# Kernel optimization log

Hardware: AMD Instinct MI355X
Metric: run time of the kernel (lower is better)

The kernel has to match this reference:

```python
import jax, jax.numpy as jnp
import numpy as np

# Dimensions (see shape_source)
B, N, F = 2, 400, 246          # batch, nodes, node features
S = 1                           # edge feature channels
C = 32                          # stack_channels
LBL = 1440                      # shape_node_labels
STACK_IN = 2 * F + 2 * S        # concat([x_i, x_j, e_ij, e_ji])
NODE_IN = F + 2 * C             # concat([x, agg_in, agg_out])


def _glorot(key, shape):
    fan_in, fan_out = shape[0], shape[1]
    lim = np.sqrt(6.0 / (fan_in + fan_out)).astype(np.float32)
    return jax.random.uniform(key, shape, jnp.float32, -lim, lim)


def setup_inputs() -> dict:
    key = jax.random.key(0)
    ks = jax.random.split(key, 12)
    x = jax.random.normal(ks[0], (B, N, F), jnp.float32)
    a = (jax.random.uniform(ks[1], (B, N, N)) < 0.10).astype(jnp.float32)
    e = jax.random.uniform(ks[2], (B, N, N, S), jnp.float32)
    return {
        "x": x,
        "a": a,
        "e": e,
        # XENetConv stack model: single Dense(C) + PReLU (per-channel alpha)
        "W_stack": _glorot(ks[3], (STACK_IN, C)),
        "b_stack": jnp.zeros((C,), jnp.float32),
        "alpha": jnp.full((C,), 0.25, jnp.float32),
        # attention heads: Dense(1, sigmoid) each
        "W_att_i": _glorot(ks[4], (C, 1)),
        "b_att_i": jnp.zeros((1,), jnp.float32),
        "W_att_j": _glorot(ks[5], (C, 1)),
        "b_att_j": jnp.zeros((1,), jnp.float32),
        # node model: Dense(F) over concat([x, agg_in, agg_out]) (linear)
        "W_node": _glorot(ks[6], (NODE_IN, F)),
        "b_node": jnp.zeros((F,), jnp.float32),
        # trailing Dense(shape_node_labels, linear)
        "W_out": _glorot(ks[7], (F, LBL)),
        "b_out": jnp.zeros((LBL,), jnp.float32),
    }


def reference(x, a, e, W_stack, b_stack, alpha, W_att_i, b_att_i,
              W_att_j, b_att_j, W_node, b_node, W_out, b_out):
    # --- XENetConvBatch ---
    # pairwise stack: [x_i, x_j, e_ij, e_ji] over all (i, j) node pairs
    x_i = jnp.broadcast_to(x[:, :, None, :], (B, N, N, F))
    x_j = jnp.broadcast_to(x[:, None, :, :], (B, N, N, F))
    e_t = jnp.transpose(e, (0, 2, 1, 3))                     # e_ji
    stack = jnp.concatenate([x_i, x_j, e, e_t], axis=-1)     # (B,N,N,2F+2S)
    s = jnp.einsum("bijk,kc->bijc", stack, W_stack) + b_stack  # (B,N,N,C)
    s = jnp.where(s >= 0, s, alpha * s)                      # PReLU
    s = s * a[..., None]                                     # mask non-edges
    # attention (sigmoid gates for incoming / outgoing aggregation)
    att_i = jax.nn.sigmoid(s @ W_att_i + b_att_i)            # (B,N,N,1)
    att_j = jax.nn.sigmoid(s @ W_att_j + b_att_j)
    agg_i = jnp.sum(s * att_i, axis=2)                       # (B,N,C) sum over j
    agg_j = jnp.sum(s * att_j, axis=1)                       # (B,N,C) sum over i
    x_new = jnp.concatenate([x, agg_i, agg_j], axis=-1) @ W_node + b_node  # (B,N,F)
    # Net discards the edge output of the conv; final linear Dense
    out = x_new @ W_out + b_out                              # (B,N,LBL)
    return out
```

## Files before the change

kernel.cpp:

```cpp
#include <hip/hip_runtime.h>
#include <math.h>

#define B_ 2
#define N_ 400
#define F_ 246
#define C_ 32
#define LBL_ 1440
#define NODE_IN_ 310

#define KX_ 320
#define KN_ 256

#define T_ABUF (800 * KX_)
#define T_WNT  (256 * KX_)
#define T_WOT  (LBL_ * KN_)

typedef __attribute__((ext_vector_type(8))) short bf16x8;
typedef __attribute__((ext_vector_type(4))) float f32x4;

__device__ __forceinline__ short f2bf(float f) {
    unsigned u = __float_as_uint(f);
    return (short)((u + 0x7FFF + ((u >> 16) & 1)) >> 16);
}

template <int K>
__device__ __forceinline__ f32x4 mfma_tile(const short* __restrict__ A,
                                           const short* __restrict__ BT,
                                           int m0, int n0, int lane) {
    int r = lane & 15, quad = lane >> 4;
    const short* ap = A + (size_t)(m0 + r) * K + quad * 8;
    const short* bp = BT + (size_t)(n0 + r) * K + quad * 8;
    f32x4 acc = {0.f, 0.f, 0.f, 0.f};
    #pragma unroll
    for (int kk = 0; kk < K; kk += 32) {
        bf16x8 av = *(const bf16x8*)(ap + kk);
        bf16x8 bv = *(const bf16x8*)(bp + kk);
        acc = __builtin_amdgcn_mfma_f32_16x16x32_bf16(av, bv, acc, 0, 0, 0);
    }
    return acc;
}

__global__ void k_pre(const float* __restrict__ x, const float* __restrict__ Ws,
                      const float* __restrict__ Wn, const float* __restrict__ Wo,
                      float* __restrict__ PQ, short* __restrict__ Abuf,
                      short* __restrict__ WnT, short* __restrict__ WoT) {
    __shared__ short tile[32][33];
    int bx = blockIdx.x, tid = threadIdx.x;
    if (bx < 50) {
        int w = tid >> 6, lane = tid & 63;
        int m0 = bx * 16, n = w * 16 + (lane & 15);
        int r = lane & 15, quad = lane >> 4;
        const float* xrow = x + (size_t)(m0 + r) * F_;
        f32x4 acc = {0.f, 0.f, 0.f, 0.f};
        #pragma unroll
        for (int kk = 0; kk < 256; kk += 32) {
            int kb = kk + quad * 8;
            bf16x8 av, bv;
            #pragma unroll
            for (int j = 0; j < 8; ++j) {
                int k = kb + j;
                av[j] = (k < F_) ? f2bf(xrow[k]) : (short)0;
                float f = 0.f;
                if (k < F_) f = (n < C_) ? Ws[k * C_ + n]
                                         : Ws[(F_ + k) * C_ + (n - C_)];
                bv[j] = f2bf(f);
            }
            acc = __builtin_amdgcn_mfma_f32_16x16x32_bf16(av, bv, acc, 0, 0, 0);
        }
        int mb = m0 + quad * 4;
        #pragma unroll
        for (int rr = 0; rr < 4; ++rr)
            PQ[(size_t)(mb + rr) * 64 + n] = acc[rr];
        return;
    }
    bx -= 50;
    if (bx < 100) {
        int r0 = bx * 8;
        for (int idx = tid; idx < 8 * F_; idx += 256) {
            int lr = idx / F_, k = idx - lr * F_;
            Abuf[(size_t)(r0 + lr) * KX_ + k] = f2bf(x[(size_t)(r0 + lr) * F_ + k]);
        }
        return;
    }
    bx -= 100;
    int tx = tid & 31, ty = tid >> 5;
    if (bx < 360) {
        int n0 = (bx % 45) * 32, k0 = (bx / 45) * 32;
        #pragma unroll
        for (int r = 0; r < 4; ++r) {
            int k = k0 + ty + r * 8;
            tile[ty + r * 8][tx] = (k < F_) ? f2bf(Wo[k * LBL_ + n0 + tx]) : (short)0;
        }
        __syncthreads();
        #pragma unroll
        for (int r = 0; r < 4; ++r)
            WoT[(size_t)(n0 + ty + r * 8) * KN_ + k0 + tx] = tile[tx][ty + r * 8];
        return;
    }
    bx -= 360;
    {
        int n0 = (bx % 8) * 32, k0 = (bx / 8) * 32;
        #pragma unroll
        for (int r = 0; r < 4; ++r) {
            int k = k0 + ty + r * 8, n = n0 + tx;
            tile[ty + r * 8][tx] =
                (n < F_ && k < NODE_IN_) ? f2bf(Wn[k * F_ + n]) : (short)0;
        }
        __syncthreads();
        #pragma unroll
        for (int r = 0; r < 4; ++r)
            WnT[(size_t)(n0 + ty + r * 8) * KX_ + k0 + tx] = tile[tx][ty + r * 8];
    }
}

__global__ void k_agg(const float* __restrict__ a, const float* __restrict__ e,
                      const float* __restrict__ Ws, const float* __restrict__ bs,
                      const float* __restrict__ alpha,
                      const float* __restrict__ Wai, const float* __restrict__ bai,
                      const float* __restrict__ Waj, const float* __restrict__ baj,
                      const float* __restrict__ PQ, short* __restrict__ Abuf) {
    int blk  = blockIdx.x;
    int mode = (blk >= B_ * N_) ? 1 : 0;
    int row  = mode ? blk - B_ * N_ : blk;
    int b = row / N_, n = row % N_;
    int tid = threadIdx.x;
    int c = tid & 31, g = tid >> 5;

    float w3  = Ws[(2 * F_) * C_ + c];
    float w4  = Ws[(2 * F_ + 1) * C_ + c];
    float bsc = bs[c];
    float alc = alpha[c];
    float wat = mode ? Waj[c] : Wai[c];
    float bat = mode ? baj[0] : bai[0];

    float ownc = PQ[(size_t)row * 64 + (mode ? 32 : 0) + c];
    const float* oth = PQ + (size_t)b * N_ * 64 + (mode ? 0 : 32) + c;
    const float* abase = a + (size_t)b * N_ * N_;
    const float* ebase = e + (size_t)b * N_ * N_;

    float acc = 0.f;
    #pragma unroll 4
    for (int m = g; m < N_; m += 8) {
        float aij  = mode ? abase[m * N_ + n] : abase[n * N_ + m];
        float er   = ebase[n * N_ + m];
        float ec   = ebase[m * N_ + n];
        float othv = oth[(size_t)m * 64];
        if (aij != 0.f) {
            float eij = mode ? ec : er;
            float eji = mode ? er : ec;
            float raw = ownc + othv + eij * w3 + eji * w4 + bsc;
            float s = (raw >= 0.f ? raw : alc * raw) * aij;
            float t2 = s * wat;
            t2 += __shfl_xor(t2, 1, 32);
            t2 += __shfl_xor(t2, 2, 32);
            t2 += __shfl_xor(t2, 4, 32);
            t2 += __shfl_xor(t2, 8, 32);
            t2 += __shfl_xor(t2, 16, 32);
            float att = 1.f / (1.f + __expf(-(t2 + bat)));
            acc += s * att;
        }
    }
    __shared__ float part[8][C_ + 1];
    part[g][c] = acc;
    __syncthreads();
    if (tid < C_) {
        float tot = 0.f;
        #pragma unroll
        for (int gg = 0; gg < 8; ++gg) tot += part[gg][tid];
        Abuf[(size_t)row * KX_ + F_ + mode * C_ + tid] = f2bf(tot);
    }
}

__global__ __launch_bounds__(1024, 1)
void k_nodeout(const short* __restrict__ Abuf, const short* __restrict__ WnT,
               const float* __restrict__ bn, const short* __restrict__ WoT,
               const float* __restrict__ bo, float* __restrict__ out) {
    __shared__ short Xs[16][264];
    int tid = threadIdx.x;
    int w = tid >> 6, lane = tid & 63;
    int m0 = blockIdx.x * 16;
    int col = lane & 15, quad = lane >> 4;

    {
        int n0 = w * 16;
        f32x4 acc = mfma_tile<KX_>(Abuf, WnT, m0, n0, lane);
        int nn = n0 + col;
        float bv = (nn < F_) ? bn[nn] : 0.f;
        #pragma unroll
        for (int r = 0; r < 4; ++r)
            Xs[quad * 4 + r][nn] = (nn < F_) ? f2bf(acc[r] + bv) : (short)0;
    }
    __syncthreads();

    const short* xbase = &Xs[0][0];
    for (int tt = w; tt < 18; tt += 16) {
        int n0 = (blockIdx.y * 18 + tt) * 16;
        int r = lane & 15;
        const short* ap = xbase + r * 264 + quad * 8;
        const short* bp = WoT + (size_t)(n0 + r) * KN_ + quad * 8;
        f32x4 acc = {0.f, 0.f, 0.f, 0.f};
        #pragma unroll
        for (int kk = 0; kk < KN_; kk += 32) {
            bf16x8 av = *(const bf16x8*)(ap + kk);
            bf16x8 bv = *(const bf16x8*)(bp + kk);
            acc = __builtin_amdgcn_mfma_f32_16x16x32_bf16(av, bv, acc, 0, 0, 0);
        }
        int nn = n0 + col;
        float bv = bo[nn];
        #pragma unroll
        for (int rr = 0; rr < 4; ++rr)
            out[(size_t)(m0 + quad * 4 + rr) * LBL_ + nn] = acc[rr] + bv;
    }
}

extern "C" void kernel_launch(void* const* d_in, const int* in_sizes, int n_in,
                              void* d_out, int out_size, void* d_ws, size_t ws_size,
                              hipStream_t stream) {
    const float* x   = (const float*)d_in[0];
    const float* a   = (const float*)d_in[1];
    const float* e   = (const float*)d_in[2];
    const float* Ws  = (const float*)d_in[3];
    const float* bs  = (const float*)d_in[4];
    const float* al  = (const float*)d_in[5];
    const float* Wai = (const float*)d_in[6];
    const float* bai = (const float*)d_in[7];
    const float* Waj = (const float*)d_in[8];
    const float* baj = (const float*)d_in[9];
    const float* Wn  = (const float*)d_in[10];
    const float* bn  = (const float*)d_in[11];
    const float* Wo  = (const float*)d_in[12];
    const float* bo  = (const float*)d_in[13];

    float* PQ   = (float*)d_ws;
    short* Abuf = (short*)(PQ + 800 * 64);
    short* WnT  = Abuf + T_ABUF;
    short* WoT  = WnT + T_WNT;

    k_pre<<<590, 256, 0, stream>>>(x, Ws, Wn, Wo, PQ, Abuf, WnT, WoT);
    k_agg<<<2 * B_ * N_, 256, 0, stream>>>(a, e, Ws, bs, al, Wai, bai, Waj, baj,
                                           PQ, Abuf);
    k_nodeout<<<dim3(50, 5), 1024, 0, stream>>>(Abuf, WnT, bn, WoT, bo,
                                                (float*)d_out);
}
```

Before: 132.6 us.

## Split PQ projection into separate MFMA kernel and rebalance nodeout tiling

The x·W_stack projection that was computed inside the prep kernel, with per-element bf16 conversion of x and Ws, is moved to a new small MFMA kernel. That kernel reads a pre-transposed bf16 W2T and the bf16 Abuf, both produced by the prep kernel, which now uses one block per row for the x conversion. The output GEMM in k_nodeout is regridded from 5 to 6 column groups with 15 tiles per block, removing the loop in which only two waves worked on the second pass. The cost is an extra kernel launch and an additional dependency between the prep and projection stages.

After: 140.9 us. 1.06x slower.

```diff
diff --git a/kernel.cpp b/kernel.cpp
--- a/kernel.cpp
+++ b/kernel.cpp
@@ -12,6 +12,7 @@
 #define KN_ 256
 
 #define T_ABUF (800 * KX_)
+#define T_W2T  (64 * KX_)
 #define T_WNT  (256 * KX_)
 #define T_WOT  (LBL_ * KN_)
 
@@ -40,49 +41,17 @@
     return acc;
 }
 
-__global__ void k_pre(const float* __restrict__ x, const float* __restrict__ Ws,
-                      const float* __restrict__ Wn, const float* __restrict__ Wo,
-                      float* __restrict__ PQ, short* __restrict__ Abuf,
-                      short* __restrict__ WnT, short* __restrict__ WoT) {
+__global__ void k_prep(const float* __restrict__ x, const float* __restrict__ Ws,
+                       const float* __restrict__ Wn, const float* __restrict__ Wo,
+                       short* __restrict__ Abuf, short* __restrict__ W2T,
+                       short* __restrict__ WnT, short* __restrict__ WoT) {
     __shared__ short tile[32][33];
     int bx = blockIdx.x, tid = threadIdx.x;
-    if (bx < 50) {
-        int w = tid >> 6, lane = tid & 63;
-        int m0 = bx * 16, n = w * 16 + (lane & 15);
-        int r = lane & 15, quad = lane >> 4;
-        const float* xrow = x + (size_t)(m0 + r) * F_;
-        f32x4 acc = {0.f, 0.f, 0.f, 0.f};
-        #pragma unroll
-        for (int kk = 0; kk < 256; kk += 32) {
-            int kb = kk + quad * 8;
-            bf16x8 av, bv;
-            #pragma unroll
-            for (int j = 0; j < 8; ++j) {
-                int k = kb + j;
-                av[j] = (k < F_) ? f2bf(xrow[k]) : (short)0;
-                float f = 0.f;
-                if (k < F_) f = (n < C_) ? Ws[k * C_ + n]
-                                         : Ws[(F_ + k) * C_ + (n - C_)];
-                bv[j] = f2bf(f);
-            }
-            acc = __builtin_amdgcn_mfma_f32_16x16x32_bf16(av, bv, acc, 0, 0, 0);
-        }
-        int mb = m0 + quad * 4;
-        #pragma unroll
-        for (int rr = 0; rr < 4; ++rr)
-            PQ[(size_t)(mb + rr) * 64 + n] = acc[rr];
+    if (bx < 800) {
+        if (tid < F_) Abuf[bx * KX_ + tid] = f2bf(x[bx * F_ + tid]);
         return;
     }
-    bx -= 50;
-    if (bx < 100) {
-        int r0 = bx * 8;
-        for (int idx = tid; idx < 8 * F_; idx += 256) {
-            int lr = idx / F_, k = idx - lr * F_;
-            Abuf[(size_t)(r0 + lr) * KX_ + k] = f2bf(x[(size_t)(r0 + lr) * F_ + k]);
-        }
-        return;
-    }
-    bx -= 100;
+    bx -= 800;
     int tx = tid & 31, ty = tid >> 5;
     if (bx < 360) {
         int n0 = (bx % 45) * 32, k0 = (bx / 45) * 32;
@@ -98,7 +67,7 @@
         return;
     }
     bx -= 360;
-    {
+    if (bx < 80) {
         int n0 = (bx % 8) * 32, k0 = (bx / 8) * 32;
         #pragma unroll
         for (int r = 0; r < 4; ++r) {
@@ -110,7 +79,29 @@
         #pragma unroll
         for (int r = 0; r < 4; ++r)
             WnT[(size_t)(n0 + ty + r * 8) * KX_ + k0 + tx] = tile[tx][ty + r * 8];
-    }
+        return;
+    }
+    bx -= 80;
+    {
+        int t = bx * 256 + tid;
+        if (t < 64 * KX_) {
+            int n = t / KX_, k = t - n * KX_;
+            float v = 0.f;
+            if (k < F_) v = (n < C_) ? Ws[k * C_ + n] : Ws[(F_ + k) * C_ + (n - C_)];
+            W2T[t] = f2bf(v);
+        }
+    }
+}
+
+__global__ void k_pq(const short* __restrict__ Abuf, const short* __restrict__ W2T,
+                     float* __restrict__ PQ) {
+    int lane = threadIdx.x;
+    int m0 = blockIdx.x * 16, n0 = blockIdx.y * 16;
+    f32x4 acc = mfma_tile<KX_>(Abuf, W2T, m0, n0, lane);
+    int n = n0 + (lane & 15), mb = m0 + (lane >> 4) * 4;
+    #pragma unroll
+    for (int r = 0; r < 4; ++r)
+        PQ[(size_t)(mb + r) * 64 + n] = acc[r];
 }
 
 __global__ void k_agg(const float* __restrict__ a, const float* __restrict__ e,
@@ -192,11 +183,10 @@
     }
     __syncthreads();
 
-    const short* xbase = &Xs[0][0];
-    for (int tt = w; tt < 18; tt += 16) {
-        int n0 = (blockIdx.y * 18 + tt) * 16;
+    if (w < 15) {
+        int n0 = (blockIdx.y * 15 + w) * 16;
         int r = lane & 15;
-        const short* ap = xbase + r * 264 + quad * 8;
+        const short* ap = &Xs[r][quad * 8];
         const short* bp = WoT + (size_t)(n0 + r) * KN_ + quad * 8;
         f32x4 acc = {0.f, 0.f, 0.f, 0.f};
         #pragma unroll
@@ -233,12 +223,14 @@
 
     float* PQ   = (float*)d_ws;
     short* Abuf = (short*)(PQ + 800 * 64);
-    short* WnT  = Abuf + T_ABUF;
+    short* W2T  = Abuf + T_ABUF;
+    short* WnT  = W2T + T_W2T;
     short* WoT  = WnT + T_WNT;
 
-    k_pre<<<590, 256, 0, stream>>>(x, Ws, Wn, Wo, PQ, Abuf, WnT, WoT);
-    k_agg<<<2 * B_ * N_, 256, 0, stream>>>(a, e, Ws, bs, al, Wai, bai, Waj, baj,
-                                           PQ, Abuf);
-    k_nodeout<<<dim3(50, 5), 1024, 0, stream>>>(Abuf, WnT, bn, WoT, bo,
+    k_prep<<<1320, 256, 0, stream>>>(x, Ws, Wn, Wo, Abuf, W2T, WnT, WoT);
+    k_pq  <<<dim3(50, 4),  64, 0, stream>>>(Abuf, W2T, PQ);
+    k_agg <<<2 * B_ * N_, 256, 0, stream>>>(a, e, Ws, bs, al, Wai, bai, Waj, baj,
+                                            PQ, Abuf);
+    k_nodeout<<<dim3(50, 6), 1024, 0, stream>>>(Abuf, WnT, bn, WoT, bo,
                                                 (float*)d_out);
 }
```
